# Kernel tuning notes

Measured on AMD Instinct MI355X. Metric: run time of the kernel, lower is better.

Reference implementation:

```python
import jax, jax.numpy as jnp
import numpy as np

B = 65536
BASE_CW = 0.5  # constraint weight at epoch 0 (progress=0)

def setup_inputs() -> dict:
    key = jax.random.key(0)
    k1, k2 = jax.random.split(key)
    outputs = jax.random.normal(k1, (B, 81, 9), dtype=jnp.float32)
    targets = jax.random.randint(k2, (B, 81), 0, 9, dtype=jnp.int64)
    return {"outputs": outputs, "targets": targets}

def reference(outputs, targets):
    b = outputs.shape[0]
    # log-softmax over the 9 digit classes (single stable pass)
    logp = jax.nn.log_softmax(outputs, axis=2)            # (B, 81, 9)
    t = targets.reshape(-1)                               # (B*81,)
    # cross entropy (mean over all cells)
    ce = -jnp.take_along_axis(logp.reshape(-1, 9), t[:, None], axis=1).mean()
    probs = jnp.exp(logp)                                 # softmax probs
    grid = probs.reshape(b, 9, 9, 9)                      # (B, row, col, digit)
    # all 27 constraint MSEs fused: per-digit mean over (B, 9), summed over digits
    row_sums = grid.sum(axis=2)                           # (B, 9, 9)
    col_sums = grid.sum(axis=1)                           # (B, 9, 9)
    box_sums = grid.reshape(b, 3, 3, 3, 3, 9).sum(axis=(2, 4)).reshape(b, 9, 9)
    constraint_loss = (
        jnp.mean((row_sums - 1.0) ** 2, axis=(0, 1)).sum()
        + jnp.mean((col_sums - 1.0) ** 2, axis=(0, 1)).sum()
        + jnp.mean((box_sums - 1.0) ** 2, axis=(0, 1)).sum()
    ) / 27.0
    # confidence (entropy) term, masked by targets != -1
    mask = (t != -1).astype(outputs.dtype)                # (B*81,)
    conf = -(probs.reshape(-1, 9) * logp.reshape(-1, 9)).sum(axis=1)
    conf = (conf * mask).sum() / (mask.sum() + 1e-8)
    return ce + BASE_CW * constraint_loss + 0.1 * conf
```

## Files before the change

### kernel.cpp

```cpp
#include <hip/hip_runtime.h>
#include <stdint.h>

#define THREADS 64
#define SPB 4
#define NBLK (65536 / SPB)
#define NUNIT (27 * SPB)

static __global__ void sudoku_main(const float* __restrict__ outs,
                                   const int*   __restrict__ targets,
                                   float*       __restrict__ partials) {
    __shared__ __align__(16) float L[SPB * 729];
    __shared__ __align__(16) int   T[SPB * 81];

    const int lane = threadIdx.x;
    const long long board0 = (long long)blockIdx.x * SPB;
    const float* __restrict__ gsrc = outs + board0 * 729;
    const int*   __restrict__ tsrc = targets + board0 * 81;

    #pragma unroll
    for (int k = 0; k < 12; ++k) {
        const int idx = k * 64 + lane;
        if (idx < 729) {
            __builtin_amdgcn_global_load_lds(
                (const __attribute__((address_space(1))) void*)(gsrc + (size_t)idx * 4),
                (__attribute__((address_space(3))) void*)(&L[k * 256]),
                16, 0, 0);
        }
    }
    #pragma unroll
    for (int k = 0; k < 2; ++k) {
        const int idx = k * 64 + lane;
        if (idx < 81) {
            __builtin_amdgcn_global_load_lds(
                (const __attribute__((address_space(1))) void*)(tsrc + (size_t)idx * 4),
                (__attribute__((address_space(3))) void*)(&T[k * 256]),
                16, 0, 0);
        }
    }
    asm volatile("s_waitcnt vmcnt(0)" ::: "memory");

    float acc_a = 0.0f, acc_c = 0.0f;
    #pragma unroll
    for (int it = 0; it < 2; ++it) {
        const int u = it * 64 + lane;
        if (u < NUNIT) {
            const int b    = u & 3;
            const int u27  = u >> 2;
            const int type = u27 / 9;
            const int unit = u27 - type * 9;
            const int ur3  = (unit / 3) * 3;
            const int uc3  = (unit % 3) * 3;
            const float* __restrict__ Lb = &L[b * 729];
            const int*   __restrict__ Tb = &T[b * 81];

            float acc[9];
            #pragma unroll
            for (int d = 0; d < 9; ++d) acc[d] = 0.0f;

            #pragma unroll
            for (int k = 0; k < 9; ++k) {
                const int cbox = (ur3 + k / 3) * 9 + uc3 + (k % 3);
                const int c = (type == 0) ? (unit * 9 + k)
                            : ((type == 1) ? (k * 9 + unit) : cbox);
                const float* __restrict__ xp = Lb + c * 9;
                float x[9], e[9];
                #pragma unroll
                for (int i = 0; i < 9; ++i) x[i] = xp[i];
                float s = 0.0f, sx = 0.0f;
                #pragma unroll
                for (int i = 0; i < 9; ++i) {
                    e[i] = __expf(x[i]);
                    s += e[i];
                    sx = fmaf(e[i], x[i], sx);
                }
                const float inv = __builtin_amdgcn_rcpf(s);
                #pragma unroll
                for (int i = 0; i < 9; ++i) acc[i] = fmaf(e[i], inv, acc[i]);

                if (type == 0) {
                    const float xt  = xp[Tb[c]];
                    const float lse = __logf(s);
                    acc_a += (lse - xt) + 0.1f * (lse - sx * inv);
                }
            }
            #pragma unroll
            for (int d = 0; d < 9; ++d) {
                const float dd = acc[d] - 1.0f;
                acc_c = fmaf(dd, dd, acc_c);
            }
        }
    }

    const float SA = 1.0f / (65536.0f * 81.0f);
    const float SB = 0.5f / (27.0f * 65536.0f * 9.0f);
    float total = acc_a * SA + acc_c * SB;
    #pragma unroll
    for (int off = 32; off > 0; off >>= 1)
        total += __shfl_down(total, off, 64);
    if (lane == 0)
        partials[blockIdx.x] = total;
}

__launch_bounds__(256)
static __global__ void sudoku_final(const float* __restrict__ partials,
                                    float*       __restrict__ out) {
    __shared__ float wave_sums[4];
    const int tid = threadIdx.x;
    const float4* __restrict__ p4 = (const float4*)partials;
    float s = 0.0f;
    #pragma unroll 4
    for (int i = tid; i < NBLK / 4; i += 256) {
        const float4 v = p4[i];
        s += (v.x + v.y) + (v.z + v.w);
    }
    #pragma unroll
    for (int off = 32; off > 0; off >>= 1)
        s += __shfl_down(s, off, 64);
    if ((tid & 63) == 0) wave_sums[tid >> 6] = s;
    __syncthreads();
    if (tid == 0)
        out[0] = wave_sums[0] + wave_sums[1] + wave_sums[2] + wave_sums[3];
}

extern "C" void kernel_launch(void* const* d_in, const int* in_sizes, int n_in,
                              void* d_out, int out_size, void* d_ws, size_t ws_size,
                              hipStream_t stream) {
    const float* outs    = (const float*)d_in[0];
    const int*   targets = (const int*)d_in[1];
    float*       partials = (float*)d_ws;
    hipLaunchKernelGGL(sudoku_main, dim3(NBLK), dim3(THREADS), 0, stream,
                       outs, targets, partials);
    hipLaunchKernelGGL(sudoku_final, dim3(1), dim3(256), 0, stream,
                       partials, (float*)d_out);
}
```

Before: 281.3 us.

## Make main kernel persistent with double-buffered async LDS prefetch

The main kernel becomes a persistent grid of 1536 single-wave blocks. Each block loops over board sets with stride GRID and uses two LDS buffers: it issues global-to-LDS loads for the next set, then waits only for the current set with a partial vmcnt before computing. The goal is to overlap memory fetch with the softmax and constraint arithmetic, and to cut per-block launch and wait overhead. The cost is fewer resident waves per CU and double the LDS per block, which may leave less room to hide compute latency.

Result: slower. 297.9 us (+5.9%).

```diff
diff --git a/kernel.cpp b/kernel.cpp
--- a/kernel.cpp
+++ b/kernel.cpp
@@ -3,27 +3,20 @@
 
 #define THREADS 64
 #define SPB 4
-#define NBLK (65536 / SPB)
+#define NSET (65536 / SPB)
+#define GRID 1536
 #define NUNIT (27 * SPB)
 
-static __global__ void sudoku_main(const float* __restrict__ outs,
-                                   const int*   __restrict__ targets,
-                                   float*       __restrict__ partials) {
-    __shared__ __align__(16) float L[SPB * 729];
-    __shared__ __align__(16) int   T[SPB * 81];
-
-    const int lane = threadIdx.x;
-    const long long board0 = (long long)blockIdx.x * SPB;
-    const float* __restrict__ gsrc = outs + board0 * 729;
-    const int*   __restrict__ tsrc = targets + board0 * 81;
-
+__device__ __forceinline__ void issue_set(const float* __restrict__ gsrc,
+                                          const int*   __restrict__ tsrc,
+                                          float* Ldst, int* Tdst, int lane) {
     #pragma unroll
     for (int k = 0; k < 12; ++k) {
         const int idx = k * 64 + lane;
         if (idx < 729) {
             __builtin_amdgcn_global_load_lds(
                 (const __attribute__((address_space(1))) void*)(gsrc + (size_t)idx * 4),
-                (__attribute__((address_space(3))) void*)(&L[k * 256]),
+                (__attribute__((address_space(3))) void*)(Ldst + k * 256),
                 16, 0, 0);
         }
     }
@@ -33,60 +26,88 @@
         if (idx < 81) {
             __builtin_amdgcn_global_load_lds(
                 (const __attribute__((address_space(1))) void*)(tsrc + (size_t)idx * 4),
-                (__attribute__((address_space(3))) void*)(&T[k * 256]),
+                (__attribute__((address_space(3))) void*)(Tdst + k * 256),
                 16, 0, 0);
         }
     }
-    asm volatile("s_waitcnt vmcnt(0)" ::: "memory");
+}
+
+static __global__ void sudoku_main(const float* __restrict__ outs,
+                                   const int*   __restrict__ targets,
+                                   float*       __restrict__ partials) {
+    __shared__ __align__(16) float L[2][SPB * 729];
+    __shared__ __align__(16) int   T[2][SPB * 81];
+
+    const int lane = threadIdx.x;
+    const int bid  = blockIdx.x;
+    const int nset = (NSET - bid + GRID - 1) / GRID;
 
     float acc_a = 0.0f, acc_c = 0.0f;
-    #pragma unroll
-    for (int it = 0; it < 2; ++it) {
-        const int u = it * 64 + lane;
-        if (u < NUNIT) {
-            const int b    = u & 3;
-            const int u27  = u >> 2;
-            const int type = u27 / 9;
-            const int unit = u27 - type * 9;
-            const int ur3  = (unit / 3) * 3;
-            const int uc3  = (unit % 3) * 3;
-            const float* __restrict__ Lb = &L[b * 729];
-            const int*   __restrict__ Tb = &T[b * 81];
 
-            float acc[9];
-            #pragma unroll
-            for (int d = 0; d < 9; ++d) acc[d] = 0.0f;
+    issue_set(outs + (size_t)bid * (SPB * 729), targets + (size_t)bid * (SPB * 81),
+              L[0], T[0], lane);
 
-            #pragma unroll
-            for (int k = 0; k < 9; ++k) {
-                const int cbox = (ur3 + k / 3) * 9 + uc3 + (k % 3);
-                const int c = (type == 0) ? (unit * 9 + k)
-                            : ((type == 1) ? (k * 9 + unit) : cbox);
-                const float* __restrict__ xp = Lb + c * 9;
-                float x[9], e[9];
+    for (int i = 0; i < nset; ++i) {
+        if (i + 1 < nset) {
+            const size_t s = (size_t)bid + (size_t)(i + 1) * GRID;
+            issue_set(outs + s * (SPB * 729), targets + s * (SPB * 81),
+                      L[(i + 1) & 1], T[(i + 1) & 1], lane);
+            asm volatile("s_waitcnt vmcnt(14)" ::: "memory");
+        } else {
+            asm volatile("s_waitcnt vmcnt(0)" ::: "memory");
+        }
+
+        const float* __restrict__ Lb = L[i & 1];
+        const int*   __restrict__ Tb = T[i & 1];
+
+        #pragma unroll
+        for (int it = 0; it < 2; ++it) {
+            const int u = it * 64 + lane;
+            if (u < NUNIT) {
+                const int b    = u & 3;
+                const int u27  = u >> 2;
+                const int type = u27 / 9;
+                const int unit = u27 - type * 9;
+                const int ur3  = (unit / 3) * 3;
+                const int uc3  = (unit % 3) * 3;
+                const float* __restrict__ Lp = Lb + b * 729;
+                const int*   __restrict__ Tp = Tb + b * 81;
+
+                float acc[9];
                 #pragma unroll
-                for (int i = 0; i < 9; ++i) x[i] = xp[i];
-                float s = 0.0f, sx = 0.0f;
+                for (int d = 0; d < 9; ++d) acc[d] = 0.0f;
+
                 #pragma unroll
-                for (int i = 0; i < 9; ++i) {
-                    e[i] = __expf(x[i]);
-                    s += e[i];
-                    sx = fmaf(e[i], x[i], sx);
+                for (int k = 0; k < 9; ++k) {
+                    const int cbox = (ur3 + k / 3) * 9 + uc3 + (k % 3);
+                    const int c = (type == 0) ? (unit * 9 + k)
+                                : ((type == 1) ? (k * 9 + unit) : cbox);
+                    const float* __restrict__ xp = Lp + c * 9;
+                    float x[9], e[9];
+                    #pragma unroll
+                    for (int j = 0; j < 9; ++j) x[j] = xp[j];
+                    float s = 0.0f, sx = 0.0f;
+                    #pragma unroll
+                    for (int j = 0; j < 9; ++j) {
+                        e[j] = __expf(x[j]);
+                        s += e[j];
+                        sx = fmaf(e[j], x[j], sx);
+                    }
+                    const float inv = __builtin_amdgcn_rcpf(s);
+                    #pragma unroll
+                    for (int j = 0; j < 9; ++j) acc[j] = fmaf(e[j], inv, acc[j]);
+
+                    if (type == 0) {
+                        const float xt  = xp[Tp[c]];
+                        const float lse = __logf(s);
+                        acc_a += (lse - xt) + 0.1f * (lse - sx * inv);
+                    }
                 }
-                const float inv = __builtin_amdgcn_rcpf(s);
                 #pragma unroll
-                for (int i = 0; i < 9; ++i) acc[i] = fmaf(e[i], inv, acc[i]);
-
-                if (type == 0) {
-                    const float xt  = xp[Tb[c]];
-                    const float lse = __logf(s);
-                    acc_a += (lse - xt) + 0.1f * (lse - sx * inv);
+                for (int d = 0; d < 9; ++d) {
+                    const float dd = acc[d] - 1.0f;
+                    acc_c = fmaf(dd, dd, acc_c);
                 }
-            }
-            #pragma unroll
-            for (int d = 0; d < 9; ++d) {
-                const float dd = acc[d] - 1.0f;
-                acc_c = fmaf(dd, dd, acc_c);
             }
         }
     }
@@ -98,7 +119,7 @@
     for (int off = 32; off > 0; off >>= 1)
         total += __shfl_down(total, off, 64);
     if (lane == 0)
-        partials[blockIdx.x] = total;
+        partials[bid] = total;
 }
 
 __launch_bounds__(256)
@@ -108,8 +129,7 @@
     const int tid = threadIdx.x;
     const float4* __restrict__ p4 = (const float4*)partials;
     float s = 0.0f;
-    #pragma unroll 4
-    for (int i = tid; i < NBLK / 4; i += 256) {
+    for (int i = tid; i < GRID / 4; i += 256) {
         const float4 v = p4[i];
         s += (v.x + v.y) + (v.z + v.w);
     }
@@ -128,7 +148,7 @@
     const float* outs    = (const float*)d_in[0];
     const int*   targets = (const int*)d_in[1];
     float*       partials = (float*)d_ws;
-    hipLaunchKernelGGL(sudoku_main, dim3(NBLK), dim3(THREADS), 0, stream,
+    hipLaunchKernelGGL(sudoku_main, dim3(GRID), dim3(THREADS), 0, stream,
                        outs, targets, partials);
     hipLaunchKernelGGL(sudoku_final, dim3(1), dim3(256), 0, stream,
                        partials, (float*)d_out);
```
